# Optimization experiments

Measured on AMD Instinct MI355X. Metric: run time of the kernel, lower is better.

## Reference

```python
import jax, jax.numpy as jnp
import numpy as np

B, S, H = 1, 2048, 4096
NQ, NKV = 32, 8
HD = H // NQ  # 128


def _rope_tables(seq_len, head_dim, base=10000.0):
    inv_freq = 1.0 / (base ** (np.arange(0, head_dim, 2, dtype=np.float32) / head_dim))
    t = np.arange(seq_len, dtype=np.float32)
    freqs = np.outer(t, inv_freq)  # (S, HD/2)
    emb = np.concatenate([freqs, freqs], axis=-1)  # (S, HD)
    return jnp.asarray(np.cos(emb)), jnp.asarray(np.sin(emb))


def setup_inputs() -> dict:
    key = jax.random.key(0)
    ks = jax.random.split(key, 5)
    cos, sin = _rope_tables(S, HD)
    scale = 1.0 / np.sqrt(H)
    return {
        "hidden_states": jax.random.normal(ks[0], (B, S, H), dtype=jnp.float32),
        "cos": cos,
        "sin": sin,
        "wq": jax.random.normal(ks[1], (H, NQ * HD), dtype=jnp.float32) * scale,
        "wk": jax.random.normal(ks[2], (H, NKV * HD), dtype=jnp.float32) * scale,
        "wv": jax.random.normal(ks[3], (H, NKV * HD), dtype=jnp.float32) * scale,
        "wo": jax.random.normal(ks[4], (NQ * HD, H), dtype=jnp.float32) * scale,
    }


def _rotate_half(x):
    x1, x2 = jnp.split(x, 2, axis=-1)
    return jnp.concatenate([-x2, x1], axis=-1)


def reference(hidden_states, cos, sin, wq, wk, wv, wo):
    b, s, _ = hidden_states.shape
    q = (hidden_states @ wq).reshape(b, s, NQ, HD)
    k = (hidden_states @ wk).reshape(b, s, NKV, HD)
    v = (hidden_states @ wv).reshape(b, s, NKV, HD)
    c = cos[None, :, None, :]
    sn = sin[None, :, None, :]
    q = q * c + _rotate_half(q) * sn
    k = k * c + _rotate_half(k) * sn
    groups = NQ // NKV
    # GQA: compute scores per kv-head group without materially repeating K/V beyond einsum
    q = q.reshape(b, s, NKV, groups, HD)
    # scores: (b, kv_head, group, s_q, s_k)
    scores = jnp.einsum("bqhgd,bkhd->bhgqk", q, k) / jnp.sqrt(jnp.asarray(HD, q.dtype))
    causal = jnp.tril(jnp.ones((s, s), dtype=bool))
    scores = jnp.where(causal[None, None, None], scores, jnp.finfo(scores.dtype).min)
    attn = jax.nn.softmax(scores, axis=-1)
    out = jnp.einsum("bhgqk,bkhd->bqhgd", attn, v)  # (b, s, kv_h, g, d)
    out = out.reshape(b, s, NQ * HD)
    return out @ wo
```

## Files before the change

kernel.cpp:

```cpp
#include <hip/hip_runtime.h>
#include <hip/hip_bf16.h>
#include <math.h>

#define S_LEN 2048
#define HDIM  4096
#define NQ_H  32
#define NKV_H 8
#define HD_   128
#define DQ (NQ_H*HD_)
#define DKV (NKV_H*HD_)
#define NFUSE (DQ + 2*DKV)

typedef unsigned short u16;
typedef unsigned int   u32;
typedef __attribute__((ext_vector_type(8))) short short8;
typedef __attribute__((ext_vector_type(4))) float f32x4;

__device__ __forceinline__ u16 bf16_rne(float x) {
    u32 u = __float_as_uint(x);
    u = (u + 0x7FFFu + ((u >> 16) & 1u)) >> 16;
    return (u16)u;
}
__device__ __forceinline__ float bf16_to_f(u16 h) {
    return __uint_as_float(((u32)h) << 16);
}
__device__ __forceinline__ void glds16(const u16* g, u16* l) {
    __builtin_amdgcn_global_load_lds(
        (const __attribute__((address_space(1))) u32*)g,
        (__attribute__((address_space(3))) u32*)l,
        16, 0, 0);
}

__global__ __launch_bounds__(256) void cvt_bf16(const float* __restrict__ in,
                                                u16* __restrict__ out, int n) {
    int i = (blockIdx.x * 256 + threadIdx.x) * 8;
    if (i >= n) return;
    float4 a = *(const float4*)&in[i];
    float4 b = *(const float4*)&in[i + 4];
    u16 h[8];
    h[0] = bf16_rne(a.x); h[1] = bf16_rne(a.y); h[2] = bf16_rne(a.z); h[3] = bf16_rne(a.w);
    h[4] = bf16_rne(b.x); h[5] = bf16_rne(b.y); h[6] = bf16_rne(b.z); h[7] = bf16_rne(b.w);
    *(uint4*)&out[i] = *(uint4*)h;
}

__global__ __launch_bounds__(256) void add_f32(const float* __restrict__ p1,
                                               float* __restrict__ out, int n) {
    int i = (blockIdx.x * 256 + threadIdx.x) * 4;
    if (i >= n) return;
    float4 a = *(const float4*)&out[i];
    float4 b = *(const float4*)&p1[i];
    a.x += b.x; a.y += b.y; a.z += b.z; a.w += b.w;
    *(float4*)&out[i] = a;
}

__global__ __launch_bounds__(256) void cvtT_qkv(const float* __restrict__ wq,
                                                const float* __restrict__ wk,
                                                const float* __restrict__ wv,
                                                u16* __restrict__ WT) {
    __shared__ float tile[32][33];
    const int n0g = blockIdx.x * 32;
    const int k0  = blockIdx.y * 32;
    const float* W; int Nsrc, nloc0;
    if (n0g < DQ)            { W = wq; Nsrc = DQ;  nloc0 = n0g; }
    else if (n0g < DQ + DKV) { W = wk; Nsrc = DKV; nloc0 = n0g - DQ; }
    else                     { W = wv; Nsrc = DKV; nloc0 = n0g - DQ - DKV; }
    const int tx = threadIdx.x & 31;
    const int ty = threadIdx.x >> 5;
#pragma unroll
    for (int i = 0; i < 4; ++i)
        tile[ty + 8 * i][tx] = W[(size_t)(k0 + ty + 8 * i) * Nsrc + nloc0 + tx];
    __syncthreads();
#pragma unroll
    for (int i = 0; i < 4; ++i) {
        int r = ty + 8 * i;
        WT[(size_t)(n0g + r) * HDIM + k0 + tx] = bf16_rne(tile[tx][r]);
    }
}

__global__ __launch_bounds__(256) void cvtT(const float* __restrict__ W,
                                            u16* __restrict__ WT, int K, int N) {
    __shared__ float tile[32][33];
    const int n0 = blockIdx.x * 32;
    const int k0 = blockIdx.y * 32;
    const int tx = threadIdx.x & 31;
    const int ty = threadIdx.x >> 5;
#pragma unroll
    for (int i = 0; i < 4; ++i)
        tile[ty + 8 * i][tx] = W[(size_t)(k0 + ty + 8 * i) * N + n0 + tx];
    __syncthreads();
#pragma unroll
    for (int i = 0; i < 4; ++i) {
        int r = ty + 8 * i;
        WT[(size_t)(n0 + r) * K + k0 + tx] = bf16_rne(tile[tx][r]);
    }
}

#define AOFFU(par, mh) ((par) * 16384 + (mh) * 8192)
#define BOFFU(par, nh) (32768 + (par) * 16384 + (nh) * 8192)

__global__ __launch_bounds__(512, 2) void gemm_qkv256(const u16* __restrict__ A,
                                                      const u16* __restrict__ BT,
                                                      u16* __restrict__ qb,
                                                      u16* __restrict__ kb,
                                                      u16* __restrict__ vb) {
    const int K  = HDIM;
    const int NT = K / 64;
    __shared__ u16 smem[65536] __attribute__((aligned(16)));

    const int t    = threadIdx.x;
    const int w    = t >> 6;
    const int lane = t & 63;
    const int wm   = w >> 2;
    const int wn   = w & 3;
    const int fr   = lane & 15;
    const int quad = lane >> 4;
    const int m0   = blockIdx.y * 256;
    const int n0   = blockIdx.x * 256;

    const int lrow = lane >> 3;
    const int lc   = (lane & 7) ^ lrow;
    const u16* const baseA = A  + (size_t)(m0 + w * 16 + lrow) * K + lc * 8;
    const u16* const baseB = BT + (size_t)(n0 + w * 16 + lrow) * K + lc * 8;
    const int wdst = w * 1024;

    const int pc0  = (quad ^ (fr & 7)) * 8;
    const int pc1  = pc0 ^ 32;
    const int aRow = (wm * 64 + fr) * 64;
    const int bRow = (wn * 32 + fr) * 64;

    f32x4 acc[2][2][4][2];
#pragma unroll
    for (int a = 0; a < 2; ++a)
#pragma unroll
        for (int b = 0; b < 2; ++b)
#pragma unroll
            for (int c = 0; c < 4; ++c)
#pragma unroll
                for (int d = 0; d < 2; ++d) acc[a][b][c][d] = (f32x4)0.f;

    short8 ar0[4][2], ar1[4][2], br[2][2];

    auto stA = [&](int off, int tile, int mh) {
        const u16* g = baseA + (size_t)mh * 128 * K + tile * 64;
        glds16(g,                 smem + off + wdst);
        glds16(g + (size_t)8 * K, smem + off + wdst + 512);
    };
    auto stB = [&](int off, int tile, int nh) {
        const u16* g = baseB + (size_t)nh * 128 * K + tile * 64;
        glds16(g,                 smem + off + wdst);
        glds16(g + (size_t)8 * K, smem + off + wdst + 512);
    };
    auto rdA = [&](short8 (&d)[4][2], int off) {
#pragma unroll
        for (int mr = 0; mr < 4; ++mr) {
            d[mr][0] = *(const short8*)&smem[off + aRow + mr * 1024 + pc0];
            d[mr][1] = *(const short8*)&smem[off + aRow + mr * 1024 + pc1];
        }
    };
    auto rdB = [&](short8 (&d)[2][2], int off) {
#pragma unroll
        for (int nc = 0; nc < 2; ++nc) {
            d[nc][0] = *(const short8*)&smem[off + bRow + nc * 1024 + pc0];
            d[nc][1] = *(const short8*)&smem[off + bRow + nc * 1024 + pc1];
        }
    };
    auto mma = [&](short8 (&a)[4][2], short8 (&b)[2][2], f32x4 (&c)[4][2]) {
        __builtin_amdgcn_s_setprio(1);
#pragma unroll
        for (int mr = 0; mr < 4; ++mr)
#pragma unroll
            for (int nc = 0; nc < 2; ++nc) {
                c[mr][nc] = __builtin_amdgcn_mfma_f32_16x16x32_bf16(a[mr][0], b[nc][0], c[mr][nc], 0, 0, 0);
                c[mr][nc] = __builtin_amdgcn_mfma_f32_16x16x32_bf16(a[mr][1], b[nc][1], c[mr][nc], 0, 0, 0);
            }
        __builtin_amdgcn_s_setprio(0);
    };

    stA(AOFFU(0,0), 0, 0);
    stB(BOFFU(0,0), 0, 0);
    stA(AOFFU(0,1), 0, 1);
    stB(BOFFU(0,1), 0, 1);
    stA(AOFFU(1,0), 1, 0);
    stB(BOFFU(1,0), 1, 0);
    stA(AOFFU(1,1), 1, 1);
    asm volatile("s_waitcnt vmcnt(6)" ::: "memory");
    __builtin_amdgcn_s_barrier();

    for (int T = 0; T < NT; T += 2) {
        const int ts2 = (T + 2 < NT) ? T + 2 : NT - 1;
        const int ts3 = (T + 3 < NT) ? T + 3 : NT - 1;
        rdA(ar0, AOFFU(0,0));
        rdB(br,  BOFFU(0,0));
        stB(BOFFU(1,1), T + 1, 1);
        __builtin_amdgcn_s_barrier();
        asm volatile("s_waitcnt lgkmcnt(0)" ::: "memory");
        mma(ar0, br, acc[0][0]);
        __builtin_amdgcn_s_barrier();
        rdA(ar1, AOFFU(0,1));
        stA(AOFFU(0,0), ts2, 0);
        __builtin_amdgcn_s_barrier();
        asm volatile("s_waitcnt lgkmcnt(0)" ::: "memory");
        mma(ar1, br, acc[1][0]);
        __builtin_amdgcn_s_barrier();
        rdB(br, BOFFU(0,1));
        stB(BOFFU(0,0), ts2, 0);
        __builtin_amdgcn_s_barrier();
        asm volatile("s_waitcnt lgkmcnt(0)" ::: "memory");
        mma(ar1, br, acc[1][1]);
        __builtin_amdgcn_s_barrier();
        stA(AOFFU(0,1), ts2, 1);
        __builtin_amdgcn_s_barrier();
        asm volatile("s_waitcnt lgkmcnt(0)" ::: "memory");
        mma(ar0, br, acc[0][1]);
        asm volatile("s_waitcnt vmcnt(6)" ::: "memory");
        __builtin_amdgcn_s_barrier();
        rdA(ar0, AOFFU(1,0));
        rdB(br,  BOFFU(1,0));
        stB(BOFFU(0,1), ts2, 1);
        __builtin_amdgcn_s_barrier();
        asm volatile("s_waitcnt lgkmcnt(0)" ::: "memory");
        mma(ar0, br, acc[0][0]);
        __builtin_amdgcn_s_barrier();
        rdA(ar1, AOFFU(1,1));
        stA(AOFFU(1,0), ts3, 0);
        __builtin_amdgcn_s_barrier();
        asm volatile("s_waitcnt lgkmcnt(0)" ::: "memory");
        mma(ar1, br, acc[1][0]);
        __builtin_amdgcn_s_barrier();
        rdB(br, BOFFU(1,1));
        stB(BOFFU(1,0), ts3, 0);
        __builtin_amdgcn_s_barrier();
        asm volatile("s_waitcnt lgkmcnt(0)" ::: "memory");
        mma(ar1, br, acc[1][1]);
        __builtin_amdgcn_s_barrier();
        stA(AOFFU(1,1), ts3, 1);
        __builtin_amdgcn_s_barrier();
        asm volatile("s_waitcnt lgkmcnt(0)" ::: "memory");
        mma(ar0, br, acc[0][1]);
        asm volatile("s_waitcnt vmcnt(6)" ::: "memory");
        __builtin_amdgcn_s_barrier();
    }

    u16* dst; int stride, nbase;
    if (n0 < DQ)            { dst = qb; stride = DQ;  nbase = n0; }
    else if (n0 < DQ + DKV) { dst = kb; stride = DKV; nbase = n0 - DQ; }
    else                    { dst = vb; stride = DKV; nbase = n0 - DQ - DKV; }

    const int col = lane & 15;
    const int rq  = (lane >> 4) * 4;
#pragma unroll
    for (int mh = 0; mh < 2; ++mh)
#pragma unroll
        for (int nh = 0; nh < 2; ++nh)
#pragma unroll
            for (int mr = 0; mr < 4; ++mr)
#pragma unroll
                for (int nc = 0; nc < 2; ++nc)
#pragma unroll
                    for (int i = 0; i < 4; ++i)
                        dst[(size_t)(m0 + mh * 128 + wm * 64 + mr * 16 + rq + i) * stride
                            + nbase + nh * 128 + wn * 32 + nc * 16 + col] =
                            bf16_rne(acc[mh][nh][mr][nc][i]);
}

__global__ __launch_bounds__(512, 2) void gemm_out256(const u16* __restrict__ A,
                                                      const u16* __restrict__ BT,
                                                      float* __restrict__ C,
                                                      float* __restrict__ P1) {
    const int LDA = DQ;
    const int NT  = 32;
    __shared__ u16 smem[65536] __attribute__((aligned(16)));

    const int t    = threadIdx.x;
    const int w    = t >> 6;
    const int lane = t & 63;
    const int wm   = w >> 2;
    const int wn   = w & 3;
    const int fr   = lane & 15;
    const int quad = lane >> 4;
    const int m0   = blockIdx.y * 256;
    const int n0   = blockIdx.x * 256;
    const int kz   = blockIdx.z * 2048;

    const int lrow = lane >> 3;
    const int lc   = (lane & 7) ^ lrow;
    const u16* const baseA = A  + (size_t)(m0 + w * 16 + lrow) * LDA + kz + lc * 8;
    const u16* const baseB = BT + (size_t)(n0 + w * 16 + lrow) * LDA + kz + lc * 8;
    const int wdst = w * 1024;

    const int pc0  = (quad ^ (fr & 7)) * 8;
    const int pc1  = pc0 ^ 32;
    const int aRow = (wm * 64 + fr) * 64;
    const int bRow = (wn * 32 + fr) * 64;

    f32x4 acc[2][2][4][2];
#pragma unroll
    for (int a = 0; a < 2; ++a)
#pragma unroll
        for (int b = 0; b < 2; ++b)
#pragma unroll
            for (int c = 0; c < 4; ++c)
#pragma unroll
                for (int d = 0; d < 2; ++d) acc[a][b][c][d] = (f32x4)0.f;

    short8 ar0[4][2], ar1[4][2], br[2][2];

    auto stA = [&](int off, int tile, int mh) {
        const u16* g = baseA + (size_t)mh * 128 * LDA + tile * 64;
        glds16(g,                   smem + off + wdst);
        glds16(g + (size_t)8 * LDA, smem + off + wdst + 512);
    };
    auto stB = [&](int off, int tile, int nh) {
        const u16* g = baseB + (size_t)nh * 128 * LDA + tile * 64;
        glds16(g,                   smem + off + wdst);
        glds16(g + (size_t)8 * LDA, smem + off + wdst + 512);
    };
    auto rdA = [&](short8 (&d)[4][2], int off) {
#pragma unroll
        for (int mr = 0; mr < 4; ++mr) {
            d[mr][0] = *(const short8*)&smem[off + aRow + mr * 1024 + pc0];
            d[mr][1] = *(const short8*)&smem[off + aRow + mr * 1024 + pc1];
        }
    };
    auto rdB = [&](short8 (&d)[2][2], int off) {
#pragma unroll
        for (int nc = 0; nc < 2; ++nc) {
            d[nc][0] = *(const short8*)&smem[off + bRow + nc * 1024 + pc0];
            d[nc][1] = *(const short8*)&smem[off + bRow + nc * 1024 + pc1];
        }
    };
    auto mma = [&](short8 (&a)[4][2], short8 (&b)[2][2], f32x4 (&c)[4][2]) {
        __builtin_amdgcn_s_setprio(1);
#pragma unroll
        for (int mr = 0; mr < 4; ++mr)
#pragma unroll
            for (int nc = 0; nc < 2; ++nc) {
                c[mr][nc] = __builtin_amdgcn_mfma_f32_16x16x32_bf16(a[mr][0], b[nc][0], c[mr][nc], 0, 0, 0);
                c[mr][nc] = __builtin_amdgcn_mfma_f32_16x16x32_bf16(a[mr][1], b[nc][1], c[mr][nc], 0, 0, 0);
            }
        __builtin_amdgcn_s_setprio(0);
    };

    stA(AOFFU(0,0), 0, 0);
    stB(BOFFU(0,0), 0, 0);
    stA(AOFFU(0,1), 0, 1);
    stB(BOFFU(0,1), 0, 1);
    stA(AOFFU(1,0), 1, 0);
    stB(BOFFU(1,0), 1, 0);
    stA(AOFFU(1,1), 1, 1);
    asm volatile("s_waitcnt vmcnt(6)" ::: "memory");
    __builtin_amdgcn_s_barrier();

    for (int T = 0; T < NT; T += 2) {
        const int ts2 = (T + 2 < NT) ? T + 2 : NT - 1;
        const int ts3 = (T + 3 < NT) ? T + 3 : NT - 1;
        rdA(ar0, AOFFU(0,0));
        rdB(br,  BOFFU(0,0));
        stB(BOFFU(1,1), T + 1, 1);
        __builtin_amdgcn_s_barrier();
        asm volatile("s_waitcnt lgkmcnt(0)" ::: "memory");
        mma(ar0, br, acc[0][0]);
        __builtin_amdgcn_s_barrier();
        rdA(ar1, AOFFU(0,1));
        stA(AOFFU(0,0), ts2, 0);
        __builtin_amdgcn_s_barrier();
        asm volatile("s_waitcnt lgkmcnt(0)" ::: "memory");
        mma(ar1, br, acc[1][0]);
        __builtin_amdgcn_s_barrier();
        rdB(br, BOFFU(0,1));
        stB(BOFFU(0,0), ts2, 0);
        __builtin_amdgcn_s_barrier();
        asm volatile("s_waitcnt lgkmcnt(0)" ::: "memory");
        mma(ar1, br, acc[1][1]);
        __builtin_amdgcn_s_barrier();
        stA(AOFFU(0,1), ts2, 1);
        __builtin_amdgcn_s_barrier();
        asm volatile("s_waitcnt lgkmcnt(0)" ::: "memory");
        mma(ar0, br, acc[0][1]);
        asm volatile("s_waitcnt vmcnt(6)" ::: "memory");
        __builtin_amdgcn_s_barrier();
        rdA(ar0, AOFFU(1,0));
        rdB(br,  BOFFU(1,0));
        stB(BOFFU(0,1), ts2, 1);
        __builtin_amdgcn_s_barrier();
        asm volatile("s_waitcnt lgkmcnt(0)" ::: "memory");
        mma(ar0, br, acc[0][0]);
        __builtin_amdgcn_s_barrier();
        rdA(ar1, AOFFU(1,1));
        stA(AOFFU(1,0), ts3, 0);
        __builtin_amdgcn_s_barrier();
        asm volatile("s_waitcnt lgkmcnt(0)" ::: "memory");
        mma(ar1, br, acc[1][0]);
        __builtin_amdgcn_s_barrier();
        rdB(br, BOFFU(1,1));
        stB(BOFFU(1,0), ts3, 0);
        __builtin_amdgcn_s_barrier();
        asm volatile("s_waitcnt lgkmcnt(0)" ::: "memory");
        mma(ar1, br, acc[1][1]);
        __builtin_amdgcn_s_barrier();
        stA(AOFFU(1,1), ts3, 1);
        __builtin_amdgcn_s_barrier();
        asm volatile("s_waitcnt lgkmcnt(0)" ::: "memory");
        mma(ar0, br, acc[0][1]);
        asm volatile("s_waitcnt vmcnt(6)" ::: "memory");
        __builtin_amdgcn_s_barrier();
    }

    float* const dst = (blockIdx.z == 0) ? C : P1;
    const int col = lane & 15;
    const int rq  = (lane >> 4) * 4;
#pragma unroll
    for (int mh = 0; mh < 2; ++mh)
#pragma unroll
        for (int nh = 0; nh < 2; ++nh)
#pragma unroll
            for (int mr = 0; mr < 4; ++mr)
#pragma unroll
                for (int nc = 0; nc < 2; ++nc)
#pragma unroll
                    for (int i = 0; i < 4; ++i)
                        dst[(size_t)(m0 + mh * 128 + wm * 64 + mr * 16 + rq + i) * HDIM
                            + n0 + nh * 128 + wn * 32 + nc * 16 + col] =
                            acc[mh][nh][mr][nc][i];
}

__global__ __launch_bounds__(256) void rope2(u16* __restrict__ q, u16* __restrict__ k,
                                             const float* __restrict__ cosT,
                                             const float* __restrict__ sinT) {
    int idx = blockIdx.x * 256 + threadIdx.x;
    int d4   = (idx & 15) * 4;
    int rest = idx >> 4;
    int head = rest % (NQ_H + NKV_H);
    int s    = rest / (NQ_H + NKV_H);
    u16* base = (head < NQ_H)
        ? q + ((size_t)s * NQ_H + head) * HD_
        : k + ((size_t)s * NKV_H + (head - NQ_H)) * HD_;
    float4 c  = *(const float4*)&cosT[s * HD_ + d4];
    float4 sn = *(const float4*)&sinT[s * HD_ + d4];
    u16 lo[4], hi[4];
    *(uint2*)lo = *(uint2*)&base[d4];
    *(uint2*)hi = *(uint2*)&base[d4 + 64];
    float cs[4] = {c.x, c.y, c.z, c.w};
    float ss[4] = {sn.x, sn.y, sn.z, sn.w};
    u16 nlo[4], nhi[4];
#pragma unroll
    for (int j = 0; j < 4; ++j) {
        float x1 = bf16_to_f(lo[j]);
        float x2 = bf16_to_f(hi[j]);
        nlo[j] = bf16_rne(x1 * cs[j] - x2 * ss[j]);
        nhi[j] = bf16_rne(x2 * cs[j] + x1 * ss[j]);
    }
    *(uint2*)&base[d4]      = *(uint2*)nlo;
    *(uint2*)&base[d4 + 64] = *(uint2*)nhi;
}

__global__ __launch_bounds__(256) void transpose_v(const u16* __restrict__ V,
                                                   u16* __restrict__ Vt) {
    __shared__ u16 tile[64][72];
    const int s0  = blockIdx.x * 64;
    const int kvh = blockIdx.y >> 1;
    const int d0  = (blockIdx.y & 1) * 64;
    const int t = threadIdx.x;
    const int chunk = t & 7;
    const int row   = t >> 3;
#pragma unroll
    for (int p = 0; p < 2; ++p) {
        int s = row + 32 * p;
        uint4 x = *(const uint4*)&V[(size_t)(s0 + s) * DKV + kvh * HD_ + d0 + chunk * 8];
        *(uint4*)&tile[s][chunk * 8] = x;
    }
    __syncthreads();
#pragma unroll
    for (int p = 0; p < 2; ++p) {
        int d = row + 32 * p;
        u16 tmp[8];
#pragma unroll
        for (int j = 0; j < 8; ++j) tmp[j] = tile[chunk * 8 + j][d];
        *(uint4*)&Vt[(size_t)(kvh * HD_ + d0 + d) * S_LEN + s0 + chunk * 8] = *(uint4*)tmp;
    }
}

#define QSTR 136
#define PSTR 76
__global__ __launch_bounds__(512, 4) void attn_mfma(const u16* __restrict__ Q,
                                                    const u16* __restrict__ K,
                                                    const u16* __restrict__ Vt,
                                                    u16* __restrict__ O) {
    __shared__ u16 smem[26112] __attribute__((aligned(16)));
    u16* sK  = smem;
    u16* sVt = smem + 8192;
    u16* sP  = smem + 16384;
    u16* sQ  = sVt;

    const int id  = blockIdx.x;
    const int h   = id & 31;
    const int qt  = (id < 256) ? (15 - (id >> 5)) : ((id - 256) >> 5);
    const int kvh = h >> 2;
    const int q0  = qt * 128;
    const int t    = threadIdx.x;
    const int w    = t >> 6;
    const int lane = t & 63;
    const int fr   = lane & 15;
    const int quad = lane >> 4;
    const int nkt  = 2 * qt + 2;

    const float K1 = 0.12751744154f;
    const float K2 = 11.5415603267f;

    const int kRow  = t >> 3;
    const int kC    = t & 7;
    const int kLds0 = kRow * 128 + (((2 * kC + 0) ^ (kRow & 7)) * 8);
    const int kLds1 = kRow * 128 + (((2 * kC + 1) ^ (kRow & 7)) * 8);
    const u16* const kGp = K + (size_t)kRow * DKV + (size_t)kvh * HD_ + kC * 16;

    const int vRow  = t >> 2;
    const int vC    = t & 3;
    const int vLds0 = vRow * 64 + (((2 * vC + 0) ^ (vRow & 7)) * 8);
    const int vLds1 = vRow * 64 + (((2 * vC + 1) ^ (vRow & 7)) * 8);
    const u16* const vGp = Vt + ((size_t)kvh * HD_ + vRow) * S_LEN + vC * 16;

    uint4 kr0 = *(const uint4*)(kGp);
    uint4 kr1 = *(const uint4*)(kGp + 8);
    uint4 vr0 = *(const uint4*)(vGp);
    uint4 vr1 = *(const uint4*)(vGp + 8);

    {
        const int col  = t & 15;
        const int row4 = t >> 4;
#pragma unroll
        for (int p = 0; p < 4; ++p) {
            int row = row4 + 32 * p;
            uint4 xv = *(const uint4*)&Q[(size_t)(q0 + row) * DQ + h * HD_ + col * 8];
            *(uint4*)&sQ[row * QSTR + col * 8] = xv;
        }
    }
    __syncthreads();

    short8 aq[4];
#pragma unroll
    for (int ks = 0; ks < 4; ++ks)
        aq[ks] = *(const short8*)&sQ[(16 * w + fr) * QSTR + ks * 32 + quad * 8];

    float lrow[4] = {0.f, 0.f, 0.f, 0.f};
    f32x4 oacc[8];
#pragma unroll
    for (int n8 = 0; n8 < 8; ++n8) oacc[n8] = (f32x4)0.f;

    u16* const sPw   = sP + w * (16 * PSTR);
    const int  qwTop = q0 + 16 * w;

    for (int kt = 0; kt < nkt; ++kt) {
        const int k0 = kt * 64;
        __syncthreads();

        *(uint4*)&sK[kLds0]  = kr0;
        *(uint4*)&sK[kLds1]  = kr1;
        *(uint4*)&sVt[vLds0] = vr0;
        *(uint4*)&sVt[vLds1] = vr1;
        if (kt + 1 < nkt) {
            const u16* kp = kGp + (size_t)(k0 + 64) * DKV;
            kr0 = *(const uint4*)(kp);
            kr1 = *(const uint4*)(kp + 8);
            const u16* vp = vGp + (k0 + 64);
            vr0 = *(const uint4*)(vp);
            vr1 = *(const uint4*)(vp + 8);
        }
        __syncthreads();

        if (k0 <= qwTop + 15) {
            f32x4 sacc[4];
#pragma unroll
            for (int nt = 0; nt < 4; ++nt) sacc[nt] = (f32x4)0.f;
#pragma unroll
            for (int ks = 0; ks < 4; ++ks)
#pragma unroll
                for (int nt = 0; nt < 4; ++nt) {
                    const short8 bk = *(const short8*)
                        &sK[(nt * 16 + fr) * 128 + (((ks * 4 + quad) ^ (fr & 7)) * 8)];
                    sacc[nt] = __builtin_amdgcn_mfma_f32_16x16x32_bf16(aq[ks], bk, sacc[nt], 0, 0, 0);
                }

            if (k0 + 63 > qwTop) {
#pragma unroll
                for (int nt = 0; nt < 4; ++nt) {
                    int key = k0 + nt * 16 + fr;
#pragma unroll
                    for (int i = 0; i < 4; ++i)
                        if (key > qwTop + quad * 4 + i) sacc[nt][i] = -INFINITY;
                }
            }

#pragma unroll
            for (int nt = 0; nt < 4; ++nt)
#pragma unroll
                for (int i = 0; i < 4; ++i) {
                    float p = __builtin_amdgcn_exp2f(fmaf(sacc[nt][i], K1, -K2));
                    lrow[i] += p;
                    sPw[(quad * 4 + i) * PSTR + nt * 16 + fr] = bf16_rne(p);
                }

#pragma unroll
            for (int ks2 = 0; ks2 < 2; ++ks2) {
                const short8 ap = *(const short8*)&sPw[fr * PSTR + ks2 * 32 + quad * 8];
#pragma unroll
                for (int n8 = 0; n8 < 8; ++n8) {
                    const short8 bv = *(const short8*)
                        &sVt[(n8 * 16 + fr) * 64 + (((ks2 * 4 + quad) ^ (fr & 7)) * 8)];
                    oacc[n8] = __builtin_amdgcn_mfma_f32_16x16x32_bf16(ap, bv, oacc[n8], 0, 0, 0);
                }
            }
        }
    }

#pragma unroll
    for (int i = 0; i < 4; ++i) {
        lrow[i] += __shfl_xor(lrow[i], 1);
        lrow[i] += __shfl_xor(lrow[i], 2);
        lrow[i] += __shfl_xor(lrow[i], 4);
        lrow[i] += __shfl_xor(lrow[i], 8);
    }
#pragma unroll
    for (int i = 0; i < 4; ++i) {
        float inv = 1.f / lrow[i];
        size_t base = (size_t)(qwTop + quad * 4 + i) * DQ + h * HD_;
#pragma unroll
        for (int n8 = 0; n8 < 8; ++n8)
            O[base + n8 * 16 + fr] = bf16_rne(oacc[n8][i] * inv);
    }
}

extern "C" void kernel_launch(void* const* d_in, const int* in_sizes, int n_in,
                              void* d_out, int out_size, void* d_ws, size_t ws_size,
                              hipStream_t stream) {
    const float* X    = (const float*)d_in[0];
    const float* cosT = (const float*)d_in[1];
    const float* sinT = (const float*)d_in[2];
    const float* wq   = (const float*)d_in[3];
    const float* wk   = (const float*)d_in[4];
    const float* wv   = (const float*)d_in[5];
    const float* wo   = (const float*)d_in[6];
    float* out = (float*)d_out;

    const size_t SDQ  = (size_t)S_LEN * DQ;
    const size_t SDKV = (size_t)S_LEN * DKV;
    const size_t WQKV = (size_t)HDIM * NFUSE;

    u16* Xb  = (u16*)d_ws;
    u16* qb  = Xb + SDQ;
    u16* kb  = qb + SDQ;
    u16* vb  = kb + SDKV;
    u16* vtb = vb + SDKV;
    u16* aob = vtb + SDKV;
    u16* WT  = aob + SDQ;
    u16* woT = WT + WQKV;

    float* P1 = (float*)d_ws;

    dim3 blk(256);

    cvt_bf16<<<SDQ / 2048, blk, 0, stream>>>(X, Xb, (int)SDQ);
    cvtT_qkv<<<dim3(NFUSE / 32, HDIM / 32), blk, 0, stream>>>(wq, wk, wv, WT);
    cvtT<<<dim3(HDIM / 32, DQ / 32), blk, 0, stream>>>(wo, woT, DQ, HDIM);

    gemm_qkv256<<<dim3(NFUSE / 256, S_LEN / 256), dim3(512), 0, stream>>>(Xb, WT, qb, kb, vb);

    rope2<<<(S_LEN * (NQ_H + NKV_H) * 16) / 256, blk, 0, stream>>>(qb, kb, cosT, sinT);

    transpose_v<<<dim3(S_LEN / 64, NKV_H * 2), blk, 0, stream>>>(vb, vtb);

    attn_mfma<<<dim3(512), dim3(512), 0, stream>>>(qb, kb, vtb, aob);

    gemm_out256<<<dim3(HDIM / 256, S_LEN / 256, 2), dim3(512), 0, stream>>>(aob, woT, out, P1);
    add_f32<<<(S_LEN * HDIM) / 1024, blk, 0, stream>>>(P1, out, S_LEN * HDIM);
}
```

Before: 476.2 us.

## Fold wo transpose-convert into QKV GEMM grid and raise MFMA wave priority

The separate wo transpose/bf16-convert kernel is removed. The QKV GEMM grid grows from 192 to 256 blocks, and the 64 extra blocks each transpose and convert a 64-column strip of wo. The goal is to fill otherwise idle CUs with the wo conversion and save one launch. In the attention kernel, s_setprio brackets the two MFMA loops to favour waves issuing matrix ops. The risk is that the 64 transpose blocks run long serial loops of 64 iterations and could become the tail of the GEMM launch.

Result: faster. 462.0 us (-3.0%).

```diff
diff --git a/kernel.cpp b/kernel.cpp
--- a/kernel.cpp
+++ b/kernel.cpp
@@ -77,24 +77,6 @@
     }
 }
 
-__global__ __launch_bounds__(256) void cvtT(const float* __restrict__ W,
-                                            u16* __restrict__ WT, int K, int N) {
-    __shared__ float tile[32][33];
-    const int n0 = blockIdx.x * 32;
-    const int k0 = blockIdx.y * 32;
-    const int tx = threadIdx.x & 31;
-    const int ty = threadIdx.x >> 5;
-#pragma unroll
-    for (int i = 0; i < 4; ++i)
-        tile[ty + 8 * i][tx] = W[(size_t)(k0 + ty + 8 * i) * N + n0 + tx];
-    __syncthreads();
-#pragma unroll
-    for (int i = 0; i < 4; ++i) {
-        int r = ty + 8 * i;
-        WT[(size_t)(n0 + r) * K + k0 + tx] = bf16_rne(tile[tx][r]);
-    }
-}
-
 #define AOFFU(par, mh) ((par) * 16384 + (mh) * 8192)
 #define BOFFU(par, nh) (32768 + (par) * 16384 + (nh) * 8192)
 
@@ -102,20 +84,46 @@
                                                       const u16* __restrict__ BT,
                                                       u16* __restrict__ qb,
                                                       u16* __restrict__ kb,
-                                                      u16* __restrict__ vb) {
+                                                      u16* __restrict__ vb,
+                                                      const float* __restrict__ wo,
+                                                      u16* __restrict__ woT) {
     const int K  = HDIM;
     const int NT = K / 64;
     __shared__ u16 smem[65536] __attribute__((aligned(16)));
 
-    const int t    = threadIdx.x;
+    const int id = blockIdx.x;
+    const int t  = threadIdx.x;
+
+    if (id >= 192) {
+        const int b  = id - 192;
+        const int n0 = b * 64;
+        float* tile = (float*)smem;
+        const int r  = t >> 3;
+        const int c8 = (t & 7) * 8;
+        for (int k0 = 0; k0 < DQ; k0 += 64) {
+            float4 x0 = *(const float4*)&wo[(size_t)(k0 + r) * HDIM + n0 + c8];
+            float4 x1 = *(const float4*)&wo[(size_t)(k0 + r) * HDIM + n0 + c8 + 4];
+            float* tr = &tile[r * 68 + c8];
+            tr[0] = x0.x; tr[1] = x0.y; tr[2] = x0.z; tr[3] = x0.w;
+            tr[4] = x1.x; tr[5] = x1.y; tr[6] = x1.z; tr[7] = x1.w;
+            __syncthreads();
+            u16 h[8];
+#pragma unroll
+            for (int j = 0; j < 8; ++j) h[j] = bf16_rne(tile[(c8 + j) * 68 + r]);
+            *(uint4*)&woT[(size_t)(n0 + r) * DQ + k0 + c8] = *(uint4*)h;
+            __syncthreads();
+        }
+        return;
+    }
+
     const int w    = t >> 6;
     const int lane = t & 63;
     const int wm   = w >> 2;
     const int wn   = w & 3;
     const int fr   = lane & 15;
     const int quad = lane >> 4;
-    const int m0   = blockIdx.y * 256;
-    const int n0   = blockIdx.x * 256;
+    const int m0   = (id / 24) * 256;
+    const int n0   = (id % 24) * 256;
 
     const int lrow = lane >> 3;
     const int lc   = (lane & 7) ^ lrow;
@@ -571,6 +579,7 @@
             f32x4 sacc[4];
 #pragma unroll
             for (int nt = 0; nt < 4; ++nt) sacc[nt] = (f32x4)0.f;
+            __builtin_amdgcn_s_setprio(1);
 #pragma unroll
             for (int ks = 0; ks < 4; ++ks)
 #pragma unroll
@@ -579,6 +588,7 @@
                         &sK[(nt * 16 + fr) * 128 + (((ks * 4 + quad) ^ (fr & 7)) * 8)];
                     sacc[nt] = __builtin_amdgcn_mfma_f32_16x16x32_bf16(aq[ks], bk, sacc[nt], 0, 0, 0);
                 }
+            __builtin_amdgcn_s_setprio(0);
 
             if (k0 + 63 > qwTop) {
 #pragma unroll
@@ -599,6 +609,7 @@
                     sPw[(quad * 4 + i) * PSTR + nt * 16 + fr] = bf16_rne(p);
                 }
 
+            __builtin_amdgcn_s_setprio(1);
 #pragma unroll
             for (int ks2 = 0; ks2 < 2; ++ks2) {
                 const short8 ap = *(const short8*)&sPw[fr * PSTR + ks2 * 32 + quad * 8];
@@ -609,6 +620,7 @@
                     oacc[n8] = __builtin_amdgcn_mfma_f32_16x16x32_bf16(ap, bv, oacc[n8], 0, 0, 0);
                 }
             }
+            __builtin_amdgcn_s_setprio(0);
         }
     }
 
@@ -660,9 +672,8 @@
 
     cvt_bf16<<<SDQ / 2048, blk, 0, stream>>>(X, Xb, (int)SDQ);
     cvtT_qkv<<<dim3(NFUSE / 32, HDIM / 32), blk, 0, stream>>>(wq, wk, wv, WT);
-    cvtT<<<dim3(HDIM / 32, DQ / 32), blk, 0, stream>>>(wo, woT, DQ, HDIM);
-
-    gemm_qkv256<<<dim3(NFUSE / 256, S_LEN / 256), dim3(512), 0, stream>>>(Xb, WT, qb, kb, vb);
+
+    gemm_qkv256<<<dim3(256), dim3(512), 0, stream>>>(Xb, WT, qb, kb, vb, wo, woT);
 
     rope2<<<(S_LEN * (NQ_H + NKV_H) * 16) / 256, blk, 0, stream>>>(qb, kb, cosT, sinT);
 
```
